# Performance work log

Hardware: AMD Instinct MI355X
Metric: run time of the kernel (lower is better)

Reference implementation:

```python
import jax, jax.numpy as jnp
import numpy as np

N = 50000      # num nodes (genes)
E = 800000     # num edges (TF->Target)
IN = 128       # in_channels
HID = 16       # hidden_channels per head
HEADS = 4
OUT = 32       # out_channels
NEG_SLOPE = 0.2  # PyG GATConv leaky_relu slope
EPS = 1e-16


def setup_inputs() -> dict:
    key = jax.random.key(0)
    ks = jax.random.split(key, 11)
    x = jax.random.normal(ks[0], (N, IN), dtype=jnp.float32)
    edge_index = jax.random.randint(ks[1], (2, E), 0, N, dtype=jnp.int32)
    # layer 1: heads=HEADS, concat=True
    W1 = jax.random.normal(ks[2], (IN, HEADS * HID), dtype=jnp.float32) * (1.0 / np.sqrt(IN))
    a_src1 = jax.random.normal(ks[3], (HEADS, HID), dtype=jnp.float32) * 0.1
    a_dst1 = jax.random.normal(ks[4], (HEADS, HID), dtype=jnp.float32) * 0.1
    b1 = jnp.zeros((HEADS * HID,), dtype=jnp.float32)
    # layer 2: heads=1, concat=False
    W2 = jax.random.normal(ks[5], (HEADS * HID, OUT), dtype=jnp.float32) * (1.0 / np.sqrt(HEADS * HID))
    a_src2 = jax.random.normal(ks[6], (1, OUT), dtype=jnp.float32) * 0.1
    a_dst2 = jax.random.normal(ks[7], (1, OUT), dtype=jnp.float32) * 0.1
    b2 = jnp.zeros((OUT,), dtype=jnp.float32)
    return dict(x=x, edge_index=edge_index, W1=W1, a_src1=a_src1, a_dst1=a_dst1, b1=b1,
                W2=W2, a_src2=a_src2, a_dst2=a_dst2, b2=b2)


def gat_layer(x, edge_index, W, a_src, a_dst, b, concat):
    """PyG GATConv (no self-loops, eval mode): gather -> edge attention -> segment softmax -> scatter."""
    n = x.shape[0]
    heads, ch = a_src.shape
    h = (x @ W).reshape(n, heads, ch)                      # [N, H, C]
    alpha_s = jnp.einsum('nhc,hc->nh', h, a_src)           # [N, H]
    alpha_d = jnp.einsum('nhc,hc->nh', h, a_dst)           # [N, H]
    src, dst = edge_index[0], edge_index[1]
    e = jax.nn.leaky_relu(alpha_s[src] + alpha_d[dst], negative_slope=NEG_SLOPE)  # [E, H]
    # numerically stable softmax over incoming edges of each dst node
    m = jax.ops.segment_max(e, dst, num_segments=n)        # [N, H]
    e = jnp.exp(e - m[dst])
    denom = jax.ops.segment_sum(e, dst, num_segments=n)    # [N, H]
    alpha = e / (denom[dst] + EPS)                         # [E, H]
    msg = h[src] * alpha[:, :, None]                       # [E, H, C]
    out = jax.ops.segment_sum(msg, dst, num_segments=n)    # [N, H, C]
    if concat:
        out = out.reshape(n, heads * ch)
    else:
        out = out.mean(axis=1)
    return out + b


def reference(x, edge_index, W1, a_src1, a_dst1, b1, W2, a_src2, a_dst2, b2):
    h = gat_layer(x, edge_index, W1, a_src1, a_dst1, b1, concat=True)   # [N, HEADS*HID]
    h = jax.nn.elu(h)
    out = gat_layer(h, edge_index, W2, a_src2, a_dst2, b2, concat=False)  # [N, OUT]
    return out
```

## Files before the change

kernel.cpp:

```cpp
#include <hip/hip_runtime.h>
#include <math.h>

#define NN 50000
#define NE 800000
#define INCH 128
#define HID1 16
#define H1 4
#define C1 64
#define C2 32
#define NEG 0.2f
#define EPSF 1e-16f
#define CAP 128
#define BSH 7
#define NBKT 391
#define CAPB 3072
#define EPB 2048
#define NPB1 391
#define GB1 782

static __device__ __forceinline__ float lrelu(float v){ return v > 0.f ? v : NEG * v; }


__global__ __launch_bounds__(256) void k_part1(const int* __restrict__ ei, int* bcnt,
                                               int2* __restrict__ pairs){
    __shared__ int hist[512];
    __shared__ int scn[512];
    __shared__ int spos[512];
    __shared__ int gbase[NBKT];
    __shared__ int2 stg[EPB];
    int t = threadIdx.x;
    hist[t] = 0; hist[t + 256] = 0;
    __syncthreads();

    int e0 = blockIdx.x * EPB;
    int tot = NE - e0; if (tot > EPB) tot = EPB;
    int srcv[8], dstv[8], rnk[8], bkt[8];
    #pragma unroll
    for (int k = 0; k < 8; ++k){
        int idx = k * 256 + t;
        if (idx < tot){
            int e = e0 + idx;
            srcv[k] = ei[e];
            dstv[k] = ei[NE + e];
            bkt[k] = dstv[k] >> BSH;
            rnk[k] = atomicAdd(&hist[bkt[k]], 1);
        } else bkt[k] = -1;
    }
    __syncthreads();

    int* sA = hist; int* sB = scn;
    for (int off = 1; off < 512; off <<= 1){
        int v0 = sA[t]       + ((t       >= off) ? sA[t - off]       : 0);
        int v1 = sA[t + 256] + ((t + 256 >= off) ? sA[t + 256 - off] : 0);
        __syncthreads();
        sB[t] = v0; sB[t + 256] = v1;
        __syncthreads();
        int* tmp = sA; sA = sB; sB = tmp;
    }
    for (int b = t; b < NBKT; b += 256){
        int incl = sA[b];
        int excl = (b > 0) ? sA[b - 1] : 0;
        spos[b] = excl;
        int cnt = incl - excl;
        gbase[b] = (cnt > 0) ? atomicAdd(&bcnt[b], cnt) : 0;
    }
    __syncthreads();

    #pragma unroll
    for (int k = 0; k < 8; ++k)
        if (bkt[k] >= 0){
            int2 pr; pr.x = srcv[k]; pr.y = dstv[k];
            stg[spos[bkt[k]] + rnk[k]] = pr;
        }
    __syncthreads();

    for (int i = t; i < tot; i += 256){
        int2 pr = stg[i];
        int b = pr.y >> BSH;
        pairs[(size_t)b * CAPB + gbase[b] + (i - spos[b])] = pr;
    }
}


__global__ __launch_bounds__(256) void k_build2(
        const int2* __restrict__ pairs, const int* __restrict__ bcnt,
        int* __restrict__ rows, int* __restrict__ deg, int* __restrict__ srcs,
        const float* __restrict__ x, const float* __restrict__ W,
        const float* __restrict__ asrc, const float* __restrict__ adst,
        float* __restrict__ h, float* __restrict__ as1, float* __restrict__ ad1){
    __shared__ __align__(16) char smem[76288];
    int t = threadIdx.x;

    if (blockIdx.x < NBKT){
        int2* stg = (int2*)smem;
        int* hist = (int*)(smem + 24576);
        int* scn  = (int*)(smem + 25088);
        int* cur  = (int*)(smem + 25600);
        int b = blockIdx.x;
        int n0 = b << BSH;
        int cnt = bcnt[b];
        if (t < 128) hist[t] = 0;
        __syncthreads();
        const int2* psrc = pairs + (size_t)b * CAPB;
        for (int i = t; i < cnt; i += 256){
            int2 pr = psrc[i];
            stg[i] = pr;
            atomicAdd(&hist[pr.y - n0], 1);
        }
        __syncthreads();
        int v = (t < 128) ? hist[t] : 0;
        if (t < 128) scn[t] = v;
        __syncthreads();
        for (int off = 1; off < 128; off <<= 1){
            int add = (t < 128 && t >= off) ? scn[t - off] : 0;
            __syncthreads();
            if (t < 128) scn[t] += add;
            __syncthreads();
        }
        if (t < 128){
            int base = b * CAPB + (scn[t] - v);
            cur[t] = base;
            int n = n0 + t;
            if (n < NN){ rows[n] = base; deg[n] = v; }
        }
        __syncthreads();
        for (int i = t; i < cnt; i += 256){
            int2 pr = stg[i];
            int p = atomicAdd(&cur[pr.y - n0], 1);
            srcs[p] = pr.x;
        }
    } else {
        float (*XT)[68] = (float(*)[68])smem;
        float* WS = (float*)(smem + 34816);
        float (*ps)[17] = (float(*)[17])(smem + 67584);
        float (*pd)[17] = (float(*)[17])(smem + 71936);
        int bid = blockIdx.x - NBKT;

        int nodeL = t >> 2;
        int kc = t & 3;
        int g = bid * 64 + nodeL;
        int gc = min(g, NN - 1);
        const float4* xr = (const float4*)(x + (size_t)gc * INCH);
        #pragma unroll
        for (int i = 0; i < 8; ++i){
            int k = kc * 32 + i * 4;
            float4 v = xr[k >> 2];
            XT[k + 0][nodeL] = v.x;
            XT[k + 1][nodeL] = v.y;
            XT[k + 2][nodeL] = v.z;
            XT[k + 3][nodeL] = v.w;
        }
        const float4* W4 = (const float4*)W;
        float4* WS4 = (float4*)WS;
        #pragma unroll
        for (int i = 0; i < 8; ++i) WS4[i * 256 + t] = W4[i * 256 + t];
        __syncthreads();

        int tx = t & 15, ty = t >> 4;
        int c4 = tx * 4, n4 = ty * 4;
        float acc[4][4];
        #pragma unroll
        for (int a = 0; a < 4; ++a)
            #pragma unroll
            for (int b2 = 0; b2 < 4; ++b2) acc[a][b2] = 0.f;

        #pragma unroll 8
        for (int k = 0; k < INCH; ++k){
            float4 xa = *(const float4*)&XT[k][n4];
            float4 wb = *(const float4*)&WS[k * C1 + c4];
            const float xv[4] = {xa.x, xa.y, xa.z, xa.w};
            const float wv[4] = {wb.x, wb.y, wb.z, wb.w};
            #pragma unroll
            for (int a = 0; a < 4; ++a)
                #pragma unroll
                for (int b2 = 0; b2 < 4; ++b2)
                    acc[a][b2] = fmaf(xv[a], wv[b2], acc[a][b2]);
        }

        int hd = tx >> 2;
        #pragma unroll
        for (int a = 0; a < 4; ++a){
            int n = bid * 64 + n4 + a;
            if (n < NN){
                float4 o = {acc[a][0], acc[a][1], acc[a][2], acc[a][3]};
                *(float4*)&h[(size_t)n * C1 + c4] = o;
            }
            float sa = 0.f, da = 0.f;
            #pragma unroll
            for (int b2 = 0; b2 < 4; ++b2){
                sa = fmaf(acc[a][b2], asrc[hd * HID1 + (c4 & 15) + b2], sa);
                da = fmaf(acc[a][b2], adst[hd * HID1 + (c4 & 15) + b2], da);
            }
            ps[n4 + a][tx] = sa;
            pd[n4 + a][tx] = da;
        }
        __syncthreads();
        int nd = t & 63, hh = t >> 6;
        int g2 = bid * 64 + nd;
        if (g2 < NN){
            float sa = ps[nd][hh*4+0] + ps[nd][hh*4+1] + ps[nd][hh*4+2] + ps[nd][hh*4+3];
            float da = pd[nd][hh*4+0] + pd[nd][hh*4+1] + pd[nd][hh*4+2] + pd[nd][hh*4+3];
            as1[g2 * H1 + hh] = sa;
            ad1[g2 * H1 + hh] = da;
        }
    }
}


__global__ __launch_bounds__(256) void k_aggA(
        const int* __restrict__ srcs, const int* __restrict__ rows,
        const int* __restrict__ deg, const float* __restrict__ h1,
        const float* __restrict__ as, const float* __restrict__ ad,
        const float* __restrict__ b1, const float* __restrict__ W2,
        const float* __restrict__ a2s, const float* __restrict__ a2d,
        float* __restrict__ h2, float* __restrict__ as2, float* __restrict__ ad2){
    __shared__ float vbuf[4][CAP * H1];
    __shared__ int   sbuf[4][CAP];
    __shared__ float sinv[4][4];
    __shared__ float hpT[16][65];
    __shared__ float WS[C1 * C2];
    int t = threadIdx.x;
    {
        const float4* W4 = (const float4*)W2;
        float4* WS4 = (float4*)WS;
        WS4[t] = W4[t];
        WS4[256 + t] = W4[256 + t];
    }
    int w = t >> 6, lane = t & 63;
    int hd1 = lane & 3, eb = lane >> 2;
    int hd3 = lane >> 4;
    float bv = b1[lane];

    #pragma unroll
    for (int q = 0; q < 4; ++q){
        int node = blockIdx.x * 16 + w * 4 + q;
        int start = rows[node], dg = deg[node];
        if (dg <= CAP){
            float adv = ad[node * H1 + hd1];
            float ssum = 0.f;
            for (int j = eb; j < dg; j += 16){
                int s = srcs[start + j];
                float wv = __expf(lrelu(as[s * H1 + hd1] + adv));
                vbuf[w][j * H1 + hd1] = wv;
                if (hd1 == 0) sbuf[w][j] = s;
                ssum += wv;
            }
            ssum += __shfl_xor(ssum, 4);
            ssum += __shfl_xor(ssum, 8);
            ssum += __shfl_xor(ssum, 16);
            ssum += __shfl_xor(ssum, 32);
            if (lane < 4) sinv[w][lane] = 1.f / (ssum + EPSF);
            float ac0 = 0.f, ac1 = 0.f;
            const float* hL = h1 + lane;
            int j = 0;
            for (; j + 1 < dg; j += 2){
                int s0 = sbuf[w][j], s1 = sbuf[w][j + 1];
                float w0 = vbuf[w][j * H1 + hd3], w1 = vbuf[w][(j + 1) * H1 + hd3];
                ac0 = fmaf(hL[(size_t)s0 * C1], w0, ac0);
                ac1 = fmaf(hL[(size_t)s1 * C1], w1, ac1);
            }
            if (j < dg)
                ac0 = fmaf(hL[(size_t)sbuf[w][j] * C1], vbuf[w][j * H1 + hd3], ac0);
            float o = (ac0 + ac1) * sinv[w][hd3] + bv;
            hpT[w * 4 + q][lane] = o > 0.f ? o : expm1f(o);
        } else {
            float adv = ad[node * H1 + hd3];
            float ss = 0.f, ac = 0.f;
            const float* hL = h1 + lane;
            for (int j = 0; j < dg; ++j){
                int s = srcs[start + j];
                float wv = __expf(lrelu(as[s * H1 + hd3] + adv));
                ss += wv;
                ac = fmaf(hL[(size_t)s * C1], wv, ac);
            }
            float o = ac / (ss + EPSF) + bv;
            hpT[w * 4 + q][lane] = o > 0.f ? o : expm1f(o);
        }
    }
    __syncthreads();

    int n = t >> 4, c = t & 15;
    float a0 = 0.f, a1 = 0.f;
    #pragma unroll 8
    for (int k = 0; k < C1; ++k){
        float hv = hpT[n][k];
        a0 = fmaf(hv, WS[k * C2 + c], a0);
        a1 = fmaf(hv, WS[k * C2 + c + 16], a1);
    }
    int gn = blockIdx.x * 16 + n;
    h2[(size_t)gn * C2 + c] = a0;
    h2[(size_t)gn * C2 + c + 16] = a1;
    float sa = a0 * a2s[c] + a1 * a2s[c + 16];
    float da = a0 * a2d[c] + a1 * a2d[c + 16];
    #pragma unroll
    for (int off = 8; off >= 1; off >>= 1){
        sa += __shfl_xor(sa, off);
        da += __shfl_xor(da, off);
    }
    if (c == 0){ as2[gn] = sa; ad2[gn] = da; }
}


__global__ __launch_bounds__(256) void k_agg2(
        const int* __restrict__ srcs, const int* __restrict__ rows,
        const int* __restrict__ deg, const float* __restrict__ h2,
        const float* __restrict__ as, const float* __restrict__ ad,
        const float* __restrict__ b2, float* __restrict__ out){
    __shared__ float vbuf[8][CAP];
    __shared__ int   sbuf[8][CAP];
    int sl = threadIdx.x >> 5;
    int lane = threadIdx.x & 31;
    int node = blockIdx.x * 8 + sl;
    int start = rows[node], dg = deg[node];
    float adv = ad[node];

    if (dg <= CAP){
        float ssum = 0.f;
        for (int j = lane; j < dg; j += 32){
            int s = srcs[start + j];
            float wv = __expf(lrelu(as[s] + adv));
            vbuf[sl][j] = wv;
            sbuf[sl][j] = s;
            ssum += wv;
        }
        #pragma unroll
        for (int off = 1; off < 32; off <<= 1) ssum += __shfl_xor(ssum, off);
        float inv = 1.f / (ssum + EPSF);
        float ac0 = 0.f, ac1 = 0.f;
        const float* hL = h2 + lane;
        int j = 0;
        for (; j + 1 < dg; j += 2){
            int s0 = sbuf[sl][j], s1 = sbuf[sl][j + 1];
            float w0 = vbuf[sl][j], w1 = vbuf[sl][j + 1];
            ac0 = fmaf(hL[(size_t)s0 * C2], w0, ac0);
            ac1 = fmaf(hL[(size_t)s1 * C2], w1, ac1);
        }
        if (j < dg)
            ac0 = fmaf(hL[(size_t)sbuf[sl][j] * C2], vbuf[sl][j], ac0);
        out[(size_t)node * C2 + lane] = (ac0 + ac1) * inv + b2[lane];
    } else {
        float ss = 0.f, ac = 0.f;
        const float* hL = h2 + lane;
        for (int j = 0; j < dg; ++j){
            int s = srcs[start + j];
            float wv = __expf(lrelu(as[s] + adv));
            ss += wv;
            ac = fmaf(hL[(size_t)s * C2], wv, ac);
        }
        out[(size_t)node * C2 + lane] = ac / (ss + EPSF) + b2[lane];
    }
}

extern "C" void kernel_launch(void* const* d_in, const int* in_sizes, int n_in,
                              void* d_out, int out_size, void* d_ws, size_t ws_size,
                              hipStream_t stream) {
    const float* x    = (const float*)d_in[0];
    const int*   ei   = (const int*)  d_in[1];
    const float* W1   = (const float*)d_in[2];
    const float* as1w = (const float*)d_in[3];
    const float* ad1w = (const float*)d_in[4];
    const float* b1   = (const float*)d_in[5];
    const float* W2   = (const float*)d_in[6];
    const float* as2w = (const float*)d_in[7];
    const float* ad2w = (const float*)d_in[8];
    const float* b2   = (const float*)d_in[9];
    float* out = (float*)d_out;

    float* p = (float*)d_ws;
    float* h1   = p; p += (size_t)NN * C1;
    float* as1  = p; p += (size_t)NN * H1;
    float* ad1  = p; p += (size_t)NN * H1;
    float* h2   = p; p += (size_t)NN * C2;
    float* as2  = p; p += NN;
    float* ad2  = p; p += NN;
    int* deg  = (int*)p; p += NN;
    int* rows = (int*)p; p += NN;
    int* bcnt = (int*)p; p += NBKT + 57;
    int* srcs = (int*)p; p += (size_t)NBKT * CAPB;
    int2* pairs = (int2*)p;

    dim3 B(256);
    hipMemsetAsync(bcnt, 0, NBKT * sizeof(int), stream);
    k_part1 <<<NPB1, B, 0, stream>>>(ei, bcnt, pairs);
    k_build2<<<NBKT + GB1, B, 0, stream>>>(pairs, bcnt, rows, deg, srcs,
                                           x, W1, as1w, ad1w, h1, as1, ad1);
    k_aggA  <<<NN / 16, B, 0, stream>>>(srcs, rows, deg, h1, as1, ad1, b1,
                                        W2, as2w, ad2w, h2, as2, ad2);
    k_agg2  <<<NN / 8, B, 0, stream>>>(srcs, rows, deg, h2, as2, ad2, b2, out);
}
```

Before: 198.8 us.

## Give each aggA wavefront one node and unroll gather loops by four

k_aggA now assigns one destination node per wavefront (4 nodes per block, 4x more blocks) instead of looping over four nodes per wavefront. This adds parallelism and removes the serial per-node loop. The small 64x32 projection is split across the two half-waves with a shuffle reduction. Both layer-1 and layer-2 gather loops go from 2 to 4 independent accumulators to raise memory-level parallelism. In exchange, each block reloads the 8KB W2 into shared memory for far fewer nodes, so that load is spread over less work.

```diff
diff --git a/kernel.cpp b/kernel.cpp
--- a/kernel.cpp
+++ b/kernel.cpp
@@ -217,7 +217,7 @@
     __shared__ float vbuf[4][CAP * H1];
     __shared__ int   sbuf[4][CAP];
     __shared__ float sinv[4][4];
-    __shared__ float hpT[16][65];
+    __shared__ float hpT[4][65];
     __shared__ float WS[C1 * C2];
     int t = threadIdx.x;
     {
@@ -229,75 +229,75 @@
     int w = t >> 6, lane = t & 63;
     int hd1 = lane & 3, eb = lane >> 2;
     int hd3 = lane >> 4;
+    int node = blockIdx.x * 4 + w;
+    int start = rows[node], dg = deg[node];
     float bv = b1[lane];
 
-    #pragma unroll
-    for (int q = 0; q < 4; ++q){
-        int node = blockIdx.x * 16 + w * 4 + q;
-        int start = rows[node], dg = deg[node];
-        if (dg <= CAP){
-            float adv = ad[node * H1 + hd1];
-            float ssum = 0.f;
-            for (int j = eb; j < dg; j += 16){
-                int s = srcs[start + j];
-                float wv = __expf(lrelu(as[s * H1 + hd1] + adv));
-                vbuf[w][j * H1 + hd1] = wv;
-                if (hd1 == 0) sbuf[w][j] = s;
-                ssum += wv;
-            }
-            ssum += __shfl_xor(ssum, 4);
-            ssum += __shfl_xor(ssum, 8);
-            ssum += __shfl_xor(ssum, 16);
-            ssum += __shfl_xor(ssum, 32);
-            if (lane < 4) sinv[w][lane] = 1.f / (ssum + EPSF);
-            float ac0 = 0.f, ac1 = 0.f;
-            const float* hL = h1 + lane;
-            int j = 0;
-            for (; j + 1 < dg; j += 2){
-                int s0 = sbuf[w][j], s1 = sbuf[w][j + 1];
-                float w0 = vbuf[w][j * H1 + hd3], w1 = vbuf[w][(j + 1) * H1 + hd3];
-                ac0 = fmaf(hL[(size_t)s0 * C1], w0, ac0);
-                ac1 = fmaf(hL[(size_t)s1 * C1], w1, ac1);
-            }
-            if (j < dg)
-                ac0 = fmaf(hL[(size_t)sbuf[w][j] * C1], vbuf[w][j * H1 + hd3], ac0);
-            float o = (ac0 + ac1) * sinv[w][hd3] + bv;
-            hpT[w * 4 + q][lane] = o > 0.f ? o : expm1f(o);
-        } else {
-            float adv = ad[node * H1 + hd3];
-            float ss = 0.f, ac = 0.f;
-            const float* hL = h1 + lane;
-            for (int j = 0; j < dg; ++j){
-                int s = srcs[start + j];
-                float wv = __expf(lrelu(as[s * H1 + hd3] + adv));
-                ss += wv;
-                ac = fmaf(hL[(size_t)s * C1], wv, ac);
-            }
-            float o = ac / (ss + EPSF) + bv;
-            hpT[w * 4 + q][lane] = o > 0.f ? o : expm1f(o);
-        }
-    }
-    __syncthreads();
-
-    int n = t >> 4, c = t & 15;
-    float a0 = 0.f, a1 = 0.f;
+    if (dg <= CAP){
+        float adv = ad[node * H1 + hd1];
+        float ssum = 0.f;
+        for (int j = eb; j < dg; j += 16){
+            int s = srcs[start + j];
+            float wv = __expf(lrelu(as[s * H1 + hd1] + adv));
+            vbuf[w][j * H1 + hd1] = wv;
+            if (hd1 == 0) sbuf[w][j] = s;
+            ssum += wv;
+        }
+        ssum += __shfl_xor(ssum, 4);
+        ssum += __shfl_xor(ssum, 8);
+        ssum += __shfl_xor(ssum, 16);
+        ssum += __shfl_xor(ssum, 32);
+        if (lane < 4) sinv[w][lane] = 1.f / (ssum + EPSF);
+        float ac0 = 0.f, ac1 = 0.f, ac2 = 0.f, ac3 = 0.f;
+        const float* hL = h1 + lane;
+        int j = 0;
+        for (; j + 3 < dg; j += 4){
+            int s0 = sbuf[w][j], s1 = sbuf[w][j+1], s2 = sbuf[w][j+2], s3 = sbuf[w][j+3];
+            float w0 = vbuf[w][(j+0)*H1+hd3], w1 = vbuf[w][(j+1)*H1+hd3];
+            float w2 = vbuf[w][(j+2)*H1+hd3], w3 = vbuf[w][(j+3)*H1+hd3];
+            ac0 = fmaf(hL[(size_t)s0 * C1], w0, ac0);
+            ac1 = fmaf(hL[(size_t)s1 * C1], w1, ac1);
+            ac2 = fmaf(hL[(size_t)s2 * C1], w2, ac2);
+            ac3 = fmaf(hL[(size_t)s3 * C1], w3, ac3);
+        }
+        for (; j < dg; ++j)
+            ac0 = fmaf(hL[(size_t)sbuf[w][j] * C1], vbuf[w][j * H1 + hd3], ac0);
+        float o = (ac0 + ac1 + ac2 + ac3) * sinv[w][hd3] + bv;
+        hpT[w][lane] = o > 0.f ? o : expm1f(o);
+    } else {
+        float adv = ad[node * H1 + hd3];
+        float ss = 0.f, ac = 0.f;
+        const float* hL = h1 + lane;
+        for (int j = 0; j < dg; ++j){
+            int s = srcs[start + j];
+            float wv = __expf(lrelu(as[s * H1 + hd3] + adv));
+            ss += wv;
+            ac = fmaf(hL[(size_t)s * C1], wv, ac);
+        }
+        float o = ac / (ss + EPSF) + bv;
+        hpT[w][lane] = o > 0.f ? o : expm1f(o);
+    }
+    __syncthreads();
+
+    int c = lane & 31, half = lane >> 5;
+    float a = 0.f;
+    int k0 = half * 32;
     #pragma unroll 8
-    for (int k = 0; k < C1; ++k){
-        float hv = hpT[n][k];
-        a0 = fmaf(hv, WS[k * C2 + c], a0);
-        a1 = fmaf(hv, WS[k * C2 + c + 16], a1);
-    }
-    int gn = blockIdx.x * 16 + n;
-    h2[(size_t)gn * C2 + c] = a0;
-    h2[(size_t)gn * C2 + c + 16] = a1;
-    float sa = a0 * a2s[c] + a1 * a2s[c + 16];
-    float da = a0 * a2d[c] + a1 * a2d[c + 16];
-    #pragma unroll
-    for (int off = 8; off >= 1; off >>= 1){
-        sa += __shfl_xor(sa, off);
-        da += __shfl_xor(da, off);
-    }
-    if (c == 0){ as2[gn] = sa; ad2[gn] = da; }
+    for (int k = k0; k < k0 + 32; ++k)
+        a = fmaf(hpT[w][k], WS[k * C2 + c], a);
+    a += __shfl_xor(a, 32);
+    int gn = blockIdx.x * 4 + w;
+    if (half == 0){
+        h2[(size_t)gn * C2 + c] = a;
+        float sa = a * a2s[c];
+        float da = a * a2d[c];
+        #pragma unroll
+        for (int off = 16; off >= 1; off >>= 1){
+            sa += __shfl_xor(sa, off);
+            da += __shfl_xor(da, off);
+        }
+        if (c == 0){ as2[gn] = sa; ad2[gn] = da; }
+    }
 }
 
 
@@ -326,18 +326,20 @@
         #pragma unroll
         for (int off = 1; off < 32; off <<= 1) ssum += __shfl_xor(ssum, off);
         float inv = 1.f / (ssum + EPSF);
-        float ac0 = 0.f, ac1 = 0.f;
+        float ac0 = 0.f, ac1 = 0.f, ac2 = 0.f, ac3 = 0.f;
         const float* hL = h2 + lane;
         int j = 0;
-        for (; j + 1 < dg; j += 2){
-            int s0 = sbuf[sl][j], s1 = sbuf[sl][j + 1];
-            float w0 = vbuf[sl][j], w1 = vbuf[sl][j + 1];
+        for (; j + 3 < dg; j += 4){
+            int s0 = sbuf[sl][j], s1 = sbuf[sl][j+1], s2 = sbuf[sl][j+2], s3 = sbuf[sl][j+3];
+            float w0 = vbuf[sl][j], w1 = vbuf[sl][j+1], w2 = vbuf[sl][j+2], w3 = vbuf[sl][j+3];
             ac0 = fmaf(hL[(size_t)s0 * C2], w0, ac0);
             ac1 = fmaf(hL[(size_t)s1 * C2], w1, ac1);
-        }
-        if (j < dg)
+            ac2 = fmaf(hL[(size_t)s2 * C2], w2, ac2);
+            ac3 = fmaf(hL[(size_t)s3 * C2], w3, ac3);
+        }
+        for (; j < dg; ++j)
             ac0 = fmaf(hL[(size_t)sbuf[sl][j] * C2], vbuf[sl][j], ac0);
-        out[(size_t)node * C2 + lane] = (ac0 + ac1) * inv + b2[lane];
+        out[(size_t)node * C2 + lane] = (ac0 + ac1 + ac2 + ac3) * inv + b2[lane];
     } else {
         float ss = 0.f, ac = 0.f;
         const float* hL = h2 + lane;
@@ -384,7 +386,7 @@
     k_part1 <<<NPB1, B, 0, stream>>>(ei, bcnt, pairs);
     k_build2<<<NBKT + GB1, B, 0, stream>>>(pairs, bcnt, rows, deg, srcs,
                                            x, W1, as1w, ad1w, h1, as1, ad1);
-    k_aggA  <<<NN / 16, B, 0, stream>>>(srcs, rows, deg, h1, as1, ad1, b1,
-                                        W2, as2w, ad2w, h2, as2, ad2);
+    k_aggA  <<<NN / 4, B, 0, stream>>>(srcs, rows, deg, h1, as1, ad1, b1,
+                                       W2, as2w, ad2w, h2, as2, ad2);
     k_agg2  <<<NN / 8, B, 0, stream>>>(srcs, rows, deg, h2, as2, ad2, b2, out);
 }
```

Result: faster. 191.1 us (-3.9%).
